# Kernel optimization log

Hardware: AMD Instinct MI355X
Metric: run time of the kernel (lower is better)

The kernel has to match this reference:

```python
import jax, jax.numpy as jnp
import numpy as np

B, N = 8, 32768
S1, S2, K = 512, 128, 32


def _knn_idx(refs, queries, k):
    # refs: (B,S,D), queries: (B,Q,D) -> (B,Q,k) indices of k nearest refs
    d = (jnp.sum(queries * queries, -1)[:, :, None]
         - 2.0 * jnp.einsum('bqd,bsd->bqs', queries, refs)
         + jnp.sum(refs * refs, -1)[:, None, :])
    _, idx = jax.lax.top_k(-d, k)
    return idx


def _gather(feats, idx):
    # feats: (B,S,C), idx: (B,Q,k) -> (B,Q,k,C)
    return jax.vmap(lambda f, i: f[i])(feats, idx)


def _mlp(x, w1, b1, w2, b2):
    # pointwise (1x1 conv) MLP: Linear -> ReLU -> Linear
    return jnp.maximum(x @ w1 + b1, 0.0) @ w2 + b2


def _set_abstraction(coords, feats, samp_idx, k, w1, b1, w2, b2):
    centers = coords[:, samp_idx]                 # (B,S,D)
    nidx = _knn_idx(coords, centers, k)           # (B,S,k)
    groups = _gather(feats, nidx)                 # (B,S,k,C)
    h = _mlp(groups, w1, b1, w2, b2)              # (B,S,k,C_out)
    return jnp.max(h, axis=2), centers


def _feature_prop(coords_q, feats_q, coords_s, feats_s, w1, b1, w2, b2):
    nidx = _knn_idx(coords_s, coords_q, 3)        # (B,Q,3)
    interp = jnp.mean(_gather(feats_s, nidx), axis=2)  # 3-NN average (sum/3)
    return _mlp(jnp.concatenate([feats_q, interp], -1), w1, b1, w2, b2)


def setup_inputs():
    key = jax.random.key(0)
    ks = jax.random.split(key, 12)

    def w(k, shape):
        return jax.random.normal(k, shape, jnp.float32) * 0.05

    z = lambda c: jnp.zeros((c,), jnp.float32)
    return {
        'x': jax.random.normal(ks[0], (B, N, 3), jnp.float32),
        'sa1_w1': w(ks[1], (3, 64)),   'sa1_b1': z(64),
        'sa1_w2': w(ks[2], (64, 64)),  'sa1_b2': z(64),
        'sa2_w1': w(ks[3], (64, 128)), 'sa2_b1': z(128),
        'sa2_w2': w(ks[4], (128, 128)),'sa2_b2': z(128),
        'fp1_w1': w(ks[5], (192, 64)), 'fp1_b1': z(64),
        'fp1_w2': w(ks[6], (64, 64)),  'fp1_b2': z(64),
        'fp2_w1': w(ks[7], (67, 32)),  'fp2_b1': z(32),
        'fp2_w2': w(ks[8], (32, 32)),  'fp2_b2': z(32),
        'fc_w': w(ks[9], (32, 2)),     'fc_b': z(2),
    }


def reference(x, sa1_w1, sa1_b1, sa1_w2, sa1_b2,
              sa2_w1, sa2_b1, sa2_w2, sa2_b2,
              fp1_w1, fp1_b1, fp1_w2, fp1_b2,
              fp2_w1, fp2_b1, fp2_w2, fp2_b2,
              fc_w, fc_b):
    rng = np.random.default_rng(0)
    samp1 = jnp.asarray(rng.permutation(N)[:S1])   # torch.randperm analog (static)
    samp2 = jnp.asarray(rng.permutation(S1)[:S2])

    f1, s1 = _set_abstraction(x, x, samp1, K, sa1_w1, sa1_b1, sa1_w2, sa1_b2)
    f2, s2 = _set_abstraction(s1, f1, samp2, K, sa2_w1, sa2_b1, sa2_w2, sa2_b2)
    g1 = _feature_prop(s1, f1, s2, f2, fp1_w1, fp1_b1, fp1_w2, fp1_b2)   # (B,512,64)
    g2 = _feature_prop(x, x, s1, g1, fp2_w1, fp2_b1, fp2_w2, fp2_b2)     # (B,N,32)
    logits = g2 @ fc_w + fc_b                                            # (B,N,2)
    return jax.nn.log_softmax(logits, axis=-1)
```

## Files before the change

kernel.cpp:

```cpp
#include <hip/hip_runtime.h>
#include <stdint.h>

#define B_ 8
#define N_ 32768
#define S1_ 512
#define S2_ 128

#define OFF_XR4   ((size_t)0)
#define OFF_C1    ((size_t)4194304)
#define OFF_C1R4  ((size_t)4243456)
#define OFF_C2    ((size_t)4308992)
#define OFF_NIDX1 ((size_t)4321280)
#define OFF_F1    ((size_t)4845568)
#define OFF_NIDX2 ((size_t)5369856)
#define OFF_F2    ((size_t)5500928)
#define OFF_G1    ((size_t)6025216)

struct Samps { int s1[S1_]; int s2[S2_]; };

typedef unsigned __int128 u128;
struct RngState { u128 state, inc; bool has32; uint32_t saved; };

static uint64_t rng_next64(RngState* r) {
  const u128 MULT = ((u128)0x2360ed051fc65da4ULL << 64) | 0x4385df649fccf645ULL;
  r->state = r->state * MULT + r->inc;
  uint64_t hi = (uint64_t)(r->state >> 64), lo = (uint64_t)r->state;
  uint64_t xs = hi ^ lo;
  unsigned rot = (unsigned)(r->state >> 122);
  return (xs >> rot) | (xs << ((64u - rot) & 63u));
}
static uint32_t rng_next32(RngState* r) {
  if (r->has32) { r->has32 = false; return r->saved; }
  uint64_t v = rng_next64(r);
  r->has32 = true; r->saved = (uint32_t)(v >> 32);
  return (uint32_t)v;
}
static uint32_t rng_interval(RngState* r, uint32_t mx) {
  if (mx == 0) return 0;
  uint32_t mask = mx;
  mask |= mask >> 1; mask |= mask >> 2; mask |= mask >> 4;
  mask |= mask >> 8; mask |= mask >> 16;
  uint32_t v;
  while ((v = (rng_next32(r) & mask)) > mx) {}
  return v;
}
static void compute_samples(int* s1, int* s2) {
  uint32_t pool[4];
  uint32_t hc = 0x43b0d7e5u;
  auto hmix = [&hc](uint32_t v) -> uint32_t {
    v ^= hc; hc *= 0x931e8875u; v *= hc; v ^= v >> 16; return v;
  };
  auto mixf = [](uint32_t x, uint32_t y) -> uint32_t {
    uint32_t rr = (x * 0xca01f9ddu) ^ (y * 0x4973f715u);
    rr ^= rr >> 16; return rr;
  };
  pool[0] = hmix(0u); pool[1] = hmix(0u); pool[2] = hmix(0u); pool[3] = hmix(0u);
  for (int s = 0; s < 4; ++s)
    for (int d = 0; d < 4; ++d)
      if (s != d) pool[d] = mixf(pool[d], hmix(pool[s]));
  uint32_t hc2 = 0x8b51f9ddu;
  uint32_t w32[8];
  for (int i = 0; i < 8; ++i) {
    uint32_t dv = pool[i & 3];
    dv ^= hc2; hc2 *= 0x58f38dedu; dv *= hc2; dv ^= dv >> 16;
    w32[i] = dv;
  }
  uint64_t w64[4];
  for (int i = 0; i < 4; ++i) w64[i] = (uint64_t)w32[2*i] | ((uint64_t)w32[2*i+1] << 32);
  const u128 MULT = ((u128)0x2360ed051fc65da4ULL << 64) | 0x4385df649fccf645ULL;
  u128 initstate = ((u128)w64[0] << 64) | w64[1];
  u128 initseq   = ((u128)w64[2] << 64) | w64[3];
  RngState r; r.has32 = false; r.saved = 0;
  r.inc = (initseq << 1) | 1;
  r.state = 0;
  r.state = r.state * MULT + r.inc;
  r.state += initstate;
  r.state = r.state * MULT + r.inc;
  static int perm1[N_];
  for (int i = 0; i < N_; ++i) perm1[i] = i;
  for (int i = N_ - 1; i > 0; --i) {
    uint32_t j = rng_interval(&r, (uint32_t)i);
    int t = perm1[i]; perm1[i] = perm1[j]; perm1[j] = t;
  }
  for (int i = 0; i < S1_; ++i) s1[i] = perm1[i];
  int perm2[S1_];
  for (int i = 0; i < S1_; ++i) perm2[i] = i;
  for (int i = S1_ - 1; i > 0; --i) {
    uint32_t j = rng_interval(&r, (uint32_t)i);
    int t = perm2[i]; perm2[i] = perm2[j]; perm2[j] = t;
  }
  for (int i = 0; i < S2_; ++i) s2[i] = perm2[i];
}


__global__ void k_prep(const float* __restrict__ x, float4* __restrict__ xr4) {
  int t = blockIdx.x * blockDim.x + threadIdx.x;
  float a = x[3*t], b = x[3*t+1], c = x[3*t+2];
  xr4[t] = make_float4(a, b, c, a*a + b*b + c*c);
}

__global__ void k_centers(const float* __restrict__ x, Samps sm,
                          float* __restrict__ c1, float4* __restrict__ c1r4,
                          float* __restrict__ c2) {
  int t = blockIdx.x * blockDim.x + threadIdx.x;
  if (t < B_*S1_) {
    int b = t >> 9, c = t & (S1_-1);
    int sidx = sm.s1[c];
    const float* src = x + ((size_t)b*N_ + sidx)*3;
    float a = src[0], bb = src[1], cc = src[2];
    c1[(size_t)t*3+0] = a; c1[(size_t)t*3+1] = bb; c1[(size_t)t*3+2] = cc;
    c1r4[t] = make_float4(a, bb, cc, a*a + bb*bb + cc*cc);
  } else {
    int u = t - B_*S1_;
    if (u < B_*S2_) {
      int b = u >> 7, c = u & (S2_-1);
      int sidx = sm.s1[sm.s2[c]];
      const float* src = x + ((size_t)b*N_ + sidx)*3;
      c2[(size_t)u*3+0] = src[0]; c2[(size_t)u*3+1] = src[1]; c2[(size_t)u*3+2] = src[2];
    }
  }
}

#define KNN_KEY(RV, UB)                                                     \
  {                                                                         \
    float dot = qx*(RV).x + qy*(RV).y + qz*(RV).z;                          \
    float dd = (qq - 2.0f*dot) + (RV).w;                                    \
    (UB) = __float_as_uint(dd);                                             \
    (UB) ^= ((unsigned int)((int)(UB) >> 31)) | 0x80000000u;                \
  }

#define KNN_DIST(RV, DD)                                                    \
  {                                                                         \
    float dot = qx*(RV).x + qy*(RV).y + qz*(RV).z;                          \
    (DD) = (qq - 2.0f*dot) + (RV).w;                                        \
  }

#define KNN_INS_F(DD, PBASE)                                                \
  {                                                                         \
    bool cand = ((DD) <= Tf);                                               \
    while (__any(cand)) {                                                   \
      unsigned long long bal = __ballot(cand);                              \
      int src = (int)__builtin_ctzll(bal);                                  \
      float df = __shfl((DD), src);                                         \
      int ii = (PBASE) + src;                                               \
      int pos = __popcll(__ballot(ldf <= df));                              \
      float ud = __shfl_up(ldf, 1);                                         \
      int ui = __shfl_up(li, 1);                                            \
      if (lane == pos)      { ldf = df; li = ii; }                          \
      else if (lane > pos)  { ldf = ud; li = ui;  }                         \
      Tf = __shfl(ldf, 31);                                                 \
      cand = cand && ((DD) <= Tf) && (lane != src);                         \
    }                                                                       \
  }

__launch_bounds__(128)
__global__ void k_knn2(const float4* __restrict__ refs4, const float* __restrict__ qpts,
                       int* __restrict__ out_idx, int nrefs, int qshift) {
  __shared__ unsigned long long kbuf[64];
  const int tid = threadIdx.x, lane = tid & 63, wv = tid >> 6;
  const int q = blockIdx.x;
  const int b = q >> qshift;
  const float4* refs = refs4 + (size_t)b * nrefs;
  const int half = nrefs >> 1;
  const int base = wv * half;
  float qx = qpts[(size_t)q*3+0], qy = qpts[(size_t)q*3+1], qz = qpts[(size_t)q*3+2];
  float qq = qx*qx + qy*qy + qz*qz;
  float ldf, Tf;
  int li;
  {
    float4 rv = refs[base + lane];
    unsigned int ub; KNN_KEY(rv, ub);
    unsigned long long key = ((unsigned long long)ub << 32) | (unsigned int)(base + lane);
    #pragma unroll
    for (int k2 = 2; k2 <= 64; k2 <<= 1) {
      #pragma unroll
      for (int j = k2 >> 1; j >= 1; j >>= 1) {
        unsigned long long o = __shfl_xor(key, j);
        bool keepmin = (((lane & j) == 0) == ((lane & k2) == 0));
        if ((o < key) == keepmin) key = o;
      }
    }
    unsigned int td = (unsigned int)(key >> 32);
    li = (int)(key & 0xffffffffu);
    int tt = (int)td >> 31;
    unsigned int mask = tt ? 0x80000000u : 0xFFFFFFFFu;
    ldf = __uint_as_float(td ^ mask);
    Tf = __shfl(ldf, 31);
  }
  {
    float4 r1 = refs[base + 64 + lane];
    float4 r2 = refs[base + 128 + lane];
    float4 r3 = refs[base + 192 + lane];
    float dd1, dd2, dd3;
    KNN_DIST(r1, dd1); KNN_DIST(r2, dd2); KNN_DIST(r3, dd3);
    KNN_INS_F(dd1, base + 64);
    KNN_INS_F(dd2, base + 128);
    KNN_INS_F(dd3, base + 192);
  }
  for (int g = base + 256; g + 255 < base + half; g += 256) {
    float4 r0 = refs[g + lane];
    float4 r1 = refs[g + 64 + lane];
    float4 r2 = refs[g + 128 + lane];
    float4 r3 = refs[g + 192 + lane];
    float dd0, dd1, dd2, dd3;
    KNN_DIST(r0, dd0); KNN_DIST(r1, dd1); KNN_DIST(r2, dd2); KNN_DIST(r3, dd3);
    KNN_INS_F(dd0, g);
    KNN_INS_F(dd1, g + 64);
    KNN_INS_F(dd2, g + 128);
    KNN_INS_F(dd3, g + 192);
  }
  {
    unsigned int ub2 = __float_as_uint(ldf);
    ub2 ^= ((unsigned int)((int)ub2 >> 31)) | 0x80000000u;
    unsigned long long key = ((unsigned long long)ub2 << 32) | (unsigned int)li;
    if (lane < 32) kbuf[wv * 32 + lane] = key;
  }
  __syncthreads();
  if (wv == 0) {
    int srcl = (lane < 32) ? lane : (95 - lane);
    unsigned long long v = kbuf[srcl];
    #pragma unroll
    for (int j = 32; j >= 1; j >>= 1) {
      unsigned long long o = __shfl_xor(v, j);
      bool keepmin = ((lane & j) == 0);
      if ((o < v) == keepmin) v = o;
    }
    if (lane < 32) out_idx[(size_t)q*32 + lane] = (int)(v & 0xffffffffu);
  }
}

__launch_bounds__(256)
__global__ void k_sa1mlp(const float* __restrict__ x, const int* __restrict__ nidx1,
                         const float* __restrict__ w1, const float* __restrict__ b1,
                         const float* __restrict__ w2, const float* __restrict__ b2,
                         float* __restrict__ f1) {
  __shared__ __align__(16) float hbuf[4][64];
  const int tid = threadIdx.x, wave = tid >> 6, lane = tid & 63;
  const int q = blockIdx.x * 4 + wave;
  const int b = q >> 9;
  const float* xb = x + (size_t)b * N_ * 3;
  float wc0 = w1[lane], wc1 = w1[64 + lane], wc2 = w1[128 + lane];
  float b1v = b1[lane], b2v = b2[lane];
  float w2c[64];
  #pragma unroll
  for (int h = 0; h < 64; ++h) w2c[h] = w2[h*64 + lane];
  const int* nb = nidx1 + (size_t)q * 32;
  int n0 = nb[0];
  float px = xb[3*n0], py = xb[3*n0+1], pz = xb[3*n0+2];
  float fm = -3.402823466e+38f;
  for (int j = 0; j < 32; ++j) {
    int n2 = nb[(j + 1) & 31];
    float nx = xb[3*n2], ny = xb[3*n2+1], nz = xb[3*n2+2];
    float h1 = fmaf(px, wc0, fmaf(py, wc1, fmaf(pz, wc2, b1v)));
    h1 = fmaxf(h1, 0.0f);
    hbuf[wave][lane] = h1;
    float acc = b2v;
    const float4* hv = (const float4*)(&hbuf[wave][0]);
    #pragma unroll
    for (int h4 = 0; h4 < 16; ++h4) {
      float4 v = hv[h4];
      acc = fmaf(v.x, w2c[4*h4+0], acc);
      acc = fmaf(v.y, w2c[4*h4+1], acc);
      acc = fmaf(v.z, w2c[4*h4+2], acc);
      acc = fmaf(v.w, w2c[4*h4+3], acc);
    }
    fm = fmaxf(fm, acc);
    px = nx; py = ny; pz = nz;
  }
  f1[(size_t)q*64 + lane] = fm;
}

__launch_bounds__(256)
__global__ void k_sa2mlp(const float* __restrict__ f1, const int* __restrict__ nidx2,
                         const float* __restrict__ w1, const float* __restrict__ b1,
                         const float* __restrict__ w2, const float* __restrict__ b2,
                         float* __restrict__ f2) {
  __shared__ __align__(16) float fin[64];
  __shared__ __align__(16) float h1s[128];
  __shared__ float ph[128];
  const int tid = threadIdx.x;
  const int s = tid >> 7, t = tid & 127;
  const int q = blockIdx.x;
  const int b = q >> 7;
  float w1r[32], w2r[64];
  #pragma unroll
  for (int i = 0; i < 32; ++i) w1r[i] = w1[(s*32 + i)*128 + t];
  #pragma unroll
  for (int h = 0; h < 64; ++h) w2r[h] = w2[(s*64 + h)*128 + t];
  float b1v = b1[t], b2v = b2[t];
  const int* nb = nidx2 + (size_t)q * 32;
  float fm = -3.402823466e+38f;
  for (int j = 0; j < 32; ++j) {
    int n = nb[j];
    __syncthreads();
    if (tid < 64) fin[tid] = f1[((size_t)b * S1_ + n)*64 + tid];
    __syncthreads();
    float p1 = 0.0f;
    const float4* fv = (const float4*)(fin + s*32);
    #pragma unroll
    for (int i4 = 0; i4 < 8; ++i4) {
      float4 v = fv[i4];
      p1 = fmaf(v.x, w1r[4*i4+0], p1);
      p1 = fmaf(v.y, w1r[4*i4+1], p1);
      p1 = fmaf(v.z, w1r[4*i4+2], p1);
      p1 = fmaf(v.w, w1r[4*i4+3], p1);
    }
    if (s) ph[t] = p1;
    __syncthreads();
    if (!s) h1s[t] = fmaxf(p1 + ph[t] + b1v, 0.0f);
    __syncthreads();
    float p2 = 0.0f;
    const float4* hv = (const float4*)(h1s + s*64);
    #pragma unroll
    for (int h4 = 0; h4 < 16; ++h4) {
      float4 v = hv[h4];
      p2 = fmaf(v.x, w2r[4*h4+0], p2);
      p2 = fmaf(v.y, w2r[4*h4+1], p2);
      p2 = fmaf(v.z, w2r[4*h4+2], p2);
      p2 = fmaf(v.w, w2r[4*h4+3], p2);
    }
    if (s) ph[t] = p2;
    __syncthreads();
    if (!s) fm = fmaxf(fm, p2 + ph[t] + b2v);
  }
  if (!s) f2[(size_t)q*128 + t] = fm;
}

__launch_bounds__(256)
__global__ void k_fp1(const float* __restrict__ c1, const float* __restrict__ c2,
                      const float* __restrict__ f1, const float* __restrict__ f2,
                      const float* __restrict__ w1, const float* __restrict__ b1,
                      const float* __restrict__ w2, const float* __restrict__ b2,
                      float* __restrict__ g1) {
  __shared__ __align__(16) float sw1[192*64];
  __shared__ __align__(16) float sw2[64*64];
  __shared__ __align__(16) float sinp[4][192];
  __shared__ __align__(16) float sh1[4][64];
  __shared__ __align__(16) float4 srefs4[S2_];
  const int tid = threadIdx.x;
  const int wave = tid >> 6, lane = tid & 63;
  const int q = blockIdx.x * 4 + wave;
  const int b = q >> 9;
  for (int i = tid; i < 192*64; i += 256) sw1[i] = w1[i];
  for (int i = tid; i < 64*64; i += 256) sw2[i] = w2[i];
  if (tid < S2_) {
    const float* rp = c2 + ((size_t)b * S2_ + tid) * 3;
    float rx = rp[0], ry = rp[1], rz = rp[2];
    srefs4[tid] = make_float4(rx, ry, rz, rx*rx + ry*ry + rz*rz);
  }
  __syncthreads();
  float qx = c1[(size_t)q*3+0], qy = c1[(size_t)q*3+1], qz = c1[(size_t)q*3+2];
  float qq = qx*qx + qy*qy + qz*qz;
  unsigned long long ka, kb;
  {
    float4 rv = srefs4[lane];
    float dot = qx*rv.x + qy*rv.y + qz*rv.z;
    float d = (qq - 2.0f*dot) + rv.w;
    unsigned int ub = __float_as_uint(d);
    ub ^= ((unsigned int)((int)ub >> 31)) | 0x80000000u;
    ka = ((unsigned long long)ub << 32) | (unsigned int)lane;
    rv = srefs4[lane + 64];
    dot = qx*rv.x + qy*rv.y + qz*rv.z;
    d = (qq - 2.0f*dot) + rv.w;
    ub = __float_as_uint(d);
    ub ^= ((unsigned int)((int)ub >> 31)) | 0x80000000u;
    kb = ((unsigned long long)ub << 32) | (unsigned int)(lane + 64);
    if (kb < ka) { unsigned long long tt = ka; ka = kb; kb = tt; }
  }
  int nsel[3];
  #pragma unroll
  for (int r = 0; r < 3; ++r) {
    unsigned long long m = ka;
    #pragma unroll
    for (int s = 1; s < 64; s <<= 1) {
      unsigned long long o = __shfl_xor(m, s);
      if (o < m) m = o;
    }
    nsel[r] = (int)(m & 0xffffffffu);
    if (ka == m) { ka = kb; kb = ~0ULL; }
  }
  const float* f2b = f2 + (size_t)b * S2_ * 128;
  sinp[wave][lane] = f1[(size_t)q*64 + lane];
  {
    float a0 = f2b[(size_t)nsel[0]*128 + lane];
    float a1 = f2b[(size_t)nsel[1]*128 + lane];
    float a2 = f2b[(size_t)nsel[2]*128 + lane];
    sinp[wave][64 + lane] = (a0 + a1 + a2) / 3.0f;
    a0 = f2b[(size_t)nsel[0]*128 + 64 + lane];
    a1 = f2b[(size_t)nsel[1]*128 + 64 + lane];
    a2 = f2b[(size_t)nsel[2]*128 + 64 + lane];
    sinp[wave][128 + lane] = (a0 + a1 + a2) / 3.0f;
  }
  __syncthreads();
  float acc = b1[lane];
  const float4* sv = (const float4*)(&sinp[wave][0]);
  #pragma unroll
  for (int i4 = 0; i4 < 48; ++i4) {
    float4 v = sv[i4];
    acc = fmaf(v.x, sw1[(4*i4+0)*64 + lane], acc);
    acc = fmaf(v.y, sw1[(4*i4+1)*64 + lane], acc);
    acc = fmaf(v.z, sw1[(4*i4+2)*64 + lane], acc);
    acc = fmaf(v.w, sw1[(4*i4+3)*64 + lane], acc);
  }
  sh1[wave][lane] = fmaxf(acc, 0.0f);
  __syncthreads();
  float acc2 = b2[lane];
  const float4* hv = (const float4*)(&sh1[wave][0]);
  #pragma unroll
  for (int h4 = 0; h4 < 16; ++h4) {
    float4 v = hv[h4];
    acc2 = fmaf(v.x, sw2[(4*h4+0)*64 + lane], acc2);
    acc2 = fmaf(v.y, sw2[(4*h4+1)*64 + lane], acc2);
    acc2 = fmaf(v.z, sw2[(4*h4+2)*64 + lane], acc2);
    acc2 = fmaf(v.w, sw2[(4*h4+3)*64 + lane], acc2);
  }
  g1[(size_t)q*64 + lane] = acc2;
}

#define FP2_PROC(RV, R)                                                     \
  {                                                                         \
    float dot = qx*(RV).x + qy*(RV).y + qz*(RV).z;                          \
    float dd = (qq - 2.0f*dot) + (RV).w;                                    \
    bool c0 = dd < d0, c1 = dd < d1, c2 = dd < d2;                          \
    i2 = c1 ? i1 : (c2 ? (R) : i2);                                         \
    d2 = c1 ? d1 : fminf(d2, dd);                                           \
    i1 = c0 ? i0 : (c1 ? (R) : i1);                                         \
    d1 = c0 ? d0 : fminf(d1, dd);                                           \
    i0 = c0 ? (R) : i0;                                                     \
    d0 = fminf(d0, dd);                                                     \
  }

__launch_bounds__(256)
__global__ void k_fp2(const float* __restrict__ x, const float4* __restrict__ c1r4,
                      const float* __restrict__ g1,
                      const float* __restrict__ w1, const float* __restrict__ b1,
                      const float* __restrict__ w2, const float* __restrict__ b2,
                      const float* __restrict__ fcw, const float* __restrict__ fcb,
                      float* __restrict__ out) {
  __shared__ __align__(16) float sw1[67*32];
  __shared__ __align__(16) float sw2[32*32];
  __shared__ __align__(16) float sfc[64];
  __shared__ float sb1[32], sb2[32], sfcb[2];
  const int tid = threadIdx.x;
  const int b = blockIdx.x >> 7;
  const int n = ((blockIdx.x & 127) << 8) + tid;
  for (int i = tid; i < 67*32; i += 256) sw1[i] = w1[i];
  for (int i = tid; i < 32*32; i += 256) sw2[i] = w2[i];
  if (tid < 64) sfc[tid] = fcw[tid];
  if (tid < 32) { sb1[tid] = b1[tid]; sb2[tid] = b2[tid]; }
  if (tid < 2) sfcb[tid] = fcb[tid];
  __syncthreads();
  const float* xb = x + (size_t)b * N_ * 3;
  float qx = xb[3*n], qy = xb[3*n+1], qz = xb[3*n+2];
  float qq = qx*qx + qy*qy + qz*qz;
  const float4* refs = c1r4 + (size_t)b * S1_;
  float d0 = 3.402823466e+38f, d1 = d0, d2 = d0;
  int i0 = 0, i1 = 0, i2 = 0;
  for (int r = 0; r < S1_; r += 4) {
    float4 ra = refs[r+0];
    float4 rb = refs[r+1];
    float4 rc = refs[r+2];
    float4 rd = refs[r+3];
    FP2_PROC(ra, r+0);
    FP2_PROC(rb, r+1);
    FP2_PROC(rc, r+2);
    FP2_PROC(rd, r+3);
  }
  const float* g1b = g1 + (size_t)b * S1_ * 64;
  const float4* p0 = (const float4*)(g1b + (size_t)i0 * 64);
  const float4* p1 = (const float4*)(g1b + (size_t)i1 * 64);
  const float4* p2 = (const float4*)(g1b + (size_t)i2 * 64);
  const float THIRD = 1.0f / 3.0f;
  float h1r[32];
  #pragma unroll
  for (int k = 0; k < 32; ++k) h1r[k] = sb1[k];
  #pragma unroll
  for (int i = 0; i < 3; ++i) {
    float v = (i == 0) ? qx : (i == 1) ? qy : qz;
    const float4* wrow = (const float4*)(sw1 + i*32);
    #pragma unroll
    for (int kq = 0; kq < 8; ++kq) {
      float4 wv = wrow[kq];
      h1r[4*kq+0] = fmaf(v, wv.x, h1r[4*kq+0]);
      h1r[4*kq+1] = fmaf(v, wv.y, h1r[4*kq+1]);
      h1r[4*kq+2] = fmaf(v, wv.z, h1r[4*kq+2]);
      h1r[4*kq+3] = fmaf(v, wv.w, h1r[4*kq+3]);
    }
  }
  #pragma unroll 4
  for (int o = 0; o < 16; ++o) {
    float4 a = p0[o], bq = p1[o], cq = p2[o];
    float vv[4];
    vv[0] = (a.x + bq.x + cq.x) * THIRD;
    vv[1] = (a.y + bq.y + cq.y) * THIRD;
    vv[2] = (a.z + bq.z + cq.z) * THIRD;
    vv[3] = (a.w + bq.w + cq.w) * THIRD;
    #pragma unroll
    for (int j = 0; j < 4; ++j) {
      float v = vv[j];
      const float4* wrow = (const float4*)(sw1 + (3 + 4*o + j)*32);
      #pragma unroll
      for (int kq = 0; kq < 8; ++kq) {
        float4 wv = wrow[kq];
        h1r[4*kq+0] = fmaf(v, wv.x, h1r[4*kq+0]);
        h1r[4*kq+1] = fmaf(v, wv.y, h1r[4*kq+1]);
        h1r[4*kq+2] = fmaf(v, wv.z, h1r[4*kq+2]);
        h1r[4*kq+3] = fmaf(v, wv.w, h1r[4*kq+3]);
      }
    }
  }
  #pragma unroll
  for (int k = 0; k < 32; ++k) h1r[k] = fmaxf(h1r[k], 0.0f);
  float h2r[32];
  #pragma unroll
  for (int m = 0; m < 32; ++m) h2r[m] = sb2[m];
  #pragma unroll
  for (int k = 0; k < 32; ++k) {
    float v = h1r[k];
    const float4* wrow = (const float4*)(sw2 + k*32);
    #pragma unroll
    for (int mq = 0; mq < 8; ++mq) {
      float4 wv = wrow[mq];
      h2r[4*mq+0] = fmaf(v, wv.x, h2r[4*mq+0]);
      h2r[4*mq+1] = fmaf(v, wv.y, h2r[4*mq+1]);
      h2r[4*mq+2] = fmaf(v, wv.z, h2r[4*mq+2]);
      h2r[4*mq+3] = fmaf(v, wv.w, h2r[4*mq+3]);
    }
  }
  float l0 = sfcb[0], l1 = sfcb[1];
  #pragma unroll
  for (int m = 0; m < 32; ++m) {
    l0 = fmaf(h2r[m], sfc[2*m+0], l0);
    l1 = fmaf(h2r[m], sfc[2*m+1], l1);
  }
  float mx = fmaxf(l0, l1);
  float s0 = l0 - mx, s1 = l1 - mx;
  float lg = logf(expf(s0) + expf(s1));
  float2 res; res.x = s0 - lg; res.y = s1 - lg;
  ((float2*)out)[(size_t)b * N_ + n] = res;
}

extern "C" void kernel_launch(void* const* d_in, const int* in_sizes, int n_in,
                              void* d_out, int out_size, void* d_ws, size_t ws_size,
                              hipStream_t stream) {
  (void)in_sizes; (void)n_in; (void)out_size; (void)ws_size;
  const float* x     = (const float*)d_in[0];
  const float* sa1w1 = (const float*)d_in[1];
  const float* sa1b1 = (const float*)d_in[2];
  const float* sa1w2 = (const float*)d_in[3];
  const float* sa1b2 = (const float*)d_in[4];
  const float* sa2w1 = (const float*)d_in[5];
  const float* sa2b1 = (const float*)d_in[6];
  const float* sa2w2 = (const float*)d_in[7];
  const float* sa2b2 = (const float*)d_in[8];
  const float* fp1w1 = (const float*)d_in[9];
  const float* fp1b1 = (const float*)d_in[10];
  const float* fp1w2 = (const float*)d_in[11];
  const float* fp1b2 = (const float*)d_in[12];
  const float* fp2w1 = (const float*)d_in[13];
  const float* fp2b1 = (const float*)d_in[14];
  const float* fp2w2 = (const float*)d_in[15];
  const float* fp2b2 = (const float*)d_in[16];
  const float* fcw   = (const float*)d_in[17];
  const float* fcb   = (const float*)d_in[18];
  float* out = (float*)d_out;
  char* ws = (char*)d_ws;
  float4* xr4  = (float4*)(ws + OFF_XR4);
  float*  c1   = (float*)(ws + OFF_C1);
  float4* c1r4 = (float4*)(ws + OFF_C1R4);
  float*  c2   = (float*)(ws + OFF_C2);
  int*    nidx1= (int*)(ws + OFF_NIDX1);
  float*  f1   = (float*)(ws + OFF_F1);
  int*    nidx2= (int*)(ws + OFF_NIDX2);
  float*  f2   = (float*)(ws + OFF_F2);
  float*  g1   = (float*)(ws + OFF_G1);

  Samps smp;
  compute_samples(smp.s1, smp.s2);

  hipLaunchKernelGGL(k_prep,    dim3(B_*N_/256), dim3(256), 0, stream, x, xr4);
  hipLaunchKernelGGL(k_centers, dim3((B_*(S1_+S2_)+255)/256), dim3(256), 0, stream,
                     x, smp, c1, c1r4, c2);
  hipLaunchKernelGGL(k_knn2,    dim3(B_*S1_), dim3(128), 0, stream, xr4, c1, nidx1, N_, 9);
  hipLaunchKernelGGL(k_sa1mlp,  dim3(B_*S1_/4), dim3(256), 0, stream,
                     x, nidx1, sa1w1, sa1b1, sa1w2, sa1b2, f1);
  hipLaunchKernelGGL(k_knn2,    dim3(B_*S2_), dim3(128), 0, stream, c1r4, c2, nidx2, S1_, 7);
  hipLaunchKernelGGL(k_sa2mlp,  dim3(B_*S2_), dim3(256), 0, stream,
                     f1, nidx2, sa2w1, sa2b1, sa2w2, sa2b2, f2);
  hipLaunchKernelGGL(k_fp1,     dim3(B_*S1_/4), dim3(256), 0, stream,
                     c1, c2, f1, f2, fp1w1, fp1b1, fp1w2, fp1b2, g1);
  hipLaunchKernelGGL(k_fp2,     dim3(B_*N_/256), dim3(256), 0, stream,
                     x, c1r4, g1, fp2w1, fp2b1, fp2w2, fp2b2, fcw, fcb, out);
}
```

Baseline: 397.7 us.

## Buffer KNN candidates in LDS and merge them in 64-wide bitonic batches

```diff
diff --git a/kernel.cpp b/kernel.cpp
--- a/kernel.cpp
+++ b/kernel.cpp
@@ -124,32 +124,63 @@
 #define KNN_KEY(RV, UB)                                                     \
   {                                                                         \
     float dot = qx*(RV).x + qy*(RV).y + qz*(RV).z;                          \
-    float dd = (qq - 2.0f*dot) + (RV).w;                                    \
-    (UB) = __float_as_uint(dd);                                             \
+    float dd_ = (qq - 2.0f*dot) + (RV).w;                                   \
+    (UB) = __float_as_uint(dd_);                                            \
     (UB) ^= ((unsigned int)((int)(UB) >> 31)) | 0x80000000u;                \
   }
 
-#define KNN_DIST(RV, DD)                                                    \
+__device__ __forceinline__ void knn_merge64(unsigned long long &lkey,
+                                            unsigned long long key, int lane) {
+  #pragma unroll
+  for (int k2 = 2; k2 <= 64; k2 <<= 1) {
+    #pragma unroll
+    for (int j = k2 >> 1; j >= 1; j >>= 1) {
+      unsigned long long o = __shfl_xor(key, j);
+      bool keepmin = (((lane & j) == 0) == ((lane & k2) == 0));
+      if ((o < key) == keepmin) key = o;
+    }
+  }
+  unsigned long long rev = __shfl(key, 63 - lane);
+  unsigned long long v = (lkey < rev) ? lkey : rev;
+  #pragma unroll
+  for (int j = 32; j >= 1; j >>= 1) {
+    unsigned long long o = __shfl_xor(v, j);
+    bool keepmin = ((lane & j) == 0);
+    if ((o < v) == keepmin) v = o;
+  }
+  lkey = v;
+}
+
+#define KNN_TUPD                                                            \
+  {                                                                         \
+    unsigned long long k31 = __shfl(lkey, 31);                              \
+    unsigned int td = (unsigned int)(k31 >> 32);                            \
+    unsigned int msk = ((int)td < 0) ? 0x80000000u : 0xFFFFFFFFu;           \
+    Tf = __uint_as_float(td ^ msk);                                         \
+  }
+
+#define KNN_CAP(RV, RIDX)                                                   \
   {                                                                         \
     float dot = qx*(RV).x + qy*(RV).y + qz*(RV).z;                          \
-    (DD) = (qq - 2.0f*dot) + (RV).w;                                        \
-  }
-
-#define KNN_INS_F(DD, PBASE)                                                \
-  {                                                                         \
-    bool cand = ((DD) <= Tf);                                               \
-    while (__any(cand)) {                                                   \
-      unsigned long long bal = __ballot(cand);                              \
-      int src = (int)__builtin_ctzll(bal);                                  \
-      float df = __shfl((DD), src);                                         \
-      int ii = (PBASE) + src;                                               \
-      int pos = __popcll(__ballot(ldf <= df));                              \
-      float ud = __shfl_up(ldf, 1);                                         \
-      int ui = __shfl_up(li, 1);                                            \
-      if (lane == pos)      { ldf = df; li = ii; }                          \
-      else if (lane > pos)  { ldf = ud; li = ui;  }                         \
-      Tf = __shfl(ldf, 31);                                                 \
-      cand = cand && ((DD) <= Tf) && (lane != src);                         \
+    float dd = (qq - 2.0f*dot) + (RV).w;                                    \
+    bool cand = (dd <= Tf);                                                 \
+    unsigned long long bal = __ballot(cand);                                \
+    if (bal) {                                                              \
+      if (cand) {                                                           \
+        int rank = __builtin_amdgcn_mbcnt_hi((unsigned int)(bal >> 32),     \
+                   __builtin_amdgcn_mbcnt_lo((unsigned int)bal, 0));        \
+        unsigned int ub = __float_as_uint(dd);                              \
+        ub ^= ((unsigned int)((int)ub >> 31)) | 0x80000000u;                \
+        cb[ccount + rank] = ((unsigned long long)ub << 32)                  \
+                          | (unsigned int)(RIDX);                           \
+      }                                                                     \
+      ccount += (int)__popcll(bal);                                         \
+      if (ccount >= 64) {                                                   \
+        unsigned long long key = cb[ccount - 64 + lane];                    \
+        knn_merge64(lkey, key, lane);                                       \
+        ccount -= 64;                                                       \
+        KNN_TUPD;                                                           \
+      }                                                                     \
     }                                                                       \
   }
 
@@ -157,6 +188,7 @@
 __global__ void k_knn2(const float4* __restrict__ refs4, const float* __restrict__ qpts,
                        int* __restrict__ out_idx, int nrefs, int qshift) {
   __shared__ unsigned long long kbuf[64];
+  __shared__ unsigned long long cbuf[2][128];
   const int tid = threadIdx.x, lane = tid & 63, wv = tid >> 6;
   const int q = blockIdx.x;
   const int b = q >> qshift;
@@ -165,56 +197,41 @@
   const int base = wv * half;
   float qx = qpts[(size_t)q*3+0], qy = qpts[(size_t)q*3+1], qz = qpts[(size_t)q*3+2];
   float qq = qx*qx + qy*qy + qz*qz;
-  float ldf, Tf;
-  int li;
+  unsigned long long lkey = ~0ULL;
+  float Tf;
+  unsigned long long* cb = &cbuf[wv][0];
+  int ccount = 0;
   {
     float4 rv = refs[base + lane];
     unsigned int ub; KNN_KEY(rv, ub);
-    unsigned long long key = ((unsigned long long)ub << 32) | (unsigned int)(base + lane);
-    #pragma unroll
-    for (int k2 = 2; k2 <= 64; k2 <<= 1) {
-      #pragma unroll
-      for (int j = k2 >> 1; j >= 1; j >>= 1) {
-        unsigned long long o = __shfl_xor(key, j);
-        bool keepmin = (((lane & j) == 0) == ((lane & k2) == 0));
-        if ((o < key) == keepmin) key = o;
-      }
-    }
-    unsigned int td = (unsigned int)(key >> 32);
-    li = (int)(key & 0xffffffffu);
-    int tt = (int)td >> 31;
-    unsigned int mask = tt ? 0x80000000u : 0xFFFFFFFFu;
-    ldf = __uint_as_float(td ^ mask);
-    Tf = __shfl(ldf, 31);
+    unsigned long long key = ((unsigned long long)ub << 32)
+                           | (unsigned int)(base + lane);
+    knn_merge64(lkey, key, lane);
+    KNN_TUPD;
   }
   {
     float4 r1 = refs[base + 64 + lane];
     float4 r2 = refs[base + 128 + lane];
     float4 r3 = refs[base + 192 + lane];
-    float dd1, dd2, dd3;
-    KNN_DIST(r1, dd1); KNN_DIST(r2, dd2); KNN_DIST(r3, dd3);
-    KNN_INS_F(dd1, base + 64);
-    KNN_INS_F(dd2, base + 128);
-    KNN_INS_F(dd3, base + 192);
+    KNN_CAP(r1, base + 64 + lane);
+    KNN_CAP(r2, base + 128 + lane);
+    KNN_CAP(r3, base + 192 + lane);
   }
   for (int g = base + 256; g + 255 < base + half; g += 256) {
     float4 r0 = refs[g + lane];
     float4 r1 = refs[g + 64 + lane];
     float4 r2 = refs[g + 128 + lane];
     float4 r3 = refs[g + 192 + lane];
-    float dd0, dd1, dd2, dd3;
-    KNN_DIST(r0, dd0); KNN_DIST(r1, dd1); KNN_DIST(r2, dd2); KNN_DIST(r3, dd3);
-    KNN_INS_F(dd0, g);
-    KNN_INS_F(dd1, g + 64);
-    KNN_INS_F(dd2, g + 128);
-    KNN_INS_F(dd3, g + 192);
+    KNN_CAP(r0, g + lane);
+    KNN_CAP(r1, g + 64 + lane);
+    KNN_CAP(r2, g + 128 + lane);
+    KNN_CAP(r3, g + 192 + lane);
   }
   {
-    unsigned int ub2 = __float_as_uint(ldf);
-    ub2 ^= ((unsigned int)((int)ub2 >> 31)) | 0x80000000u;
-    unsigned long long key = ((unsigned long long)ub2 << 32) | (unsigned int)li;
-    if (lane < 32) kbuf[wv * 32 + lane] = key;
-  }
+    unsigned long long key = (lane < ccount) ? cb[lane] : ~0ULL;
+    knn_merge64(lkey, key, lane);
+  }
+  if (lane < 32) kbuf[wv * 32 + lane] = lkey;
   __syncthreads();
   if (wv == 0) {
     int srcl = (lane < 32) ? lane : (95 - lane);
```

Result: faster. 375.3 us (-5.6%).
